# Kernel tuning notes

Hardware: AMD Instinct MI355X
Metric: run time of the kernel (lower is better)

The kernel has to match this reference:

```python
import jax, jax.numpy as jnp
import numpy as np

B, N, M, D = 8, 1024, 2048, 1024


def setup_inputs() -> dict:
    key = jax.random.key(0)
    k1, k2, k3 = jax.random.split(key, 3)
    text_features = jax.random.normal(k1, (B, N, D), dtype=jnp.float32)
    audio_features = jax.random.normal(k2, (B, M, D), dtype=jnp.float32)
    sigma = jnp.ones((1,), dtype=jnp.float32)  # learnable bandwidth, initial_sigma=1.0
    # audio lengths in [M//4, M) so no softmax row is fully masked
    audio_lengths = jnp.maximum(
        jax.random.randint(k3, (B,), 0, M), M // 4
    ).astype(jnp.int32)
    return {
        "text_features": text_features,
        "audio_features": audio_features,
        "sigma": sigma,
        "audio_lengths": audio_lengths,
    }


def reference(text_features, audio_features, sigma, audio_lengths):
    b, n, d = text_features.shape
    m = audio_features.shape[1]
    s = jnp.abs(sigma[0]) + 1e-8

    # QK^T / sqrt(d)  -> (B, N, M)
    scores = jnp.einsum("bnd,bmd->bnm", text_features, audio_features) / jnp.sqrt(
        jnp.float32(d)
    )

    # Gaussian relative positional bias: -|i/N - j/M|^2 / (2 sigma^2)
    text_pos = jnp.arange(n, dtype=jnp.float32) / n    # (N,)
    audio_pos = jnp.arange(m, dtype=jnp.float32) / m   # (M,)
    d_rel = jnp.abs(text_pos[:, None] - audio_pos[None, :])  # (N, M)
    scores = scores - d_rel**2 / (2.0 * s * s)

    # mask padded audio positions per batch element
    valid = jnp.arange(m)[None, :] < audio_lengths[:, None]  # (B, M) bool
    scores = jnp.where(valid[:, None, :], scores, -jnp.inf)

    attention_weights = jax.nn.softmax(scores, axis=-1)  # (B, N, M)
    enhanced = jnp.einsum("bnm,bmd->bnd", attention_weights, audio_features)
    return enhanced, attention_weights
```

## Files before the change

### kernel.cpp

```cpp
#include <hip/hip_runtime.h>
#include <hip/hip_bf16.h>

#define BB 8
#define NN 1024
#define MM 2048
#define DD 1024

typedef __attribute__((ext_vector_type(8))) __bf16 bfrag8;
typedef __attribute__((ext_vector_type(4))) float ffrag4;

__device__ __forceinline__ unsigned short f2bf(float f) {
  union { float f; unsigned u; } x; x.f = f;
  unsigned r = x.u + 0x7FFFu + ((x.u >> 16) & 1u);
  return (unsigned short)(r >> 16);
}

__device__ __forceinline__ void gload_lds16(const unsigned short* g, unsigned short* l) {
  __builtin_amdgcn_global_load_lds(
      (const __attribute__((address_space(1))) void*)g,
      (__attribute__((address_space(3))) void*)l, 16, 0, 0);
}


__global__ __launch_bounds__(256) void ta_cvtQ(const float* __restrict__ Q,
                                               unsigned short* __restrict__ Qbf) {
  int t = blockIdx.x * 256 + threadIdx.x;
  const float4* src = reinterpret_cast<const float4*>(Q) + t * 2;
  float4 a = src[0], b = src[1];
  ushort4 lo = { f2bf(a.x), f2bf(a.y), f2bf(a.z), f2bf(a.w) };
  ushort4 hi = { f2bf(b.x), f2bf(b.y), f2bf(b.z), f2bf(b.w) };
  ushort4* dst = reinterpret_cast<ushort4*>(Qbf) + t * 2;
  dst[0] = lo; dst[1] = hi;
}

#define TSTR 68
__global__ __launch_bounds__(256) void ta_trans(const float* __restrict__ V,
                                                unsigned short* __restrict__ Kbf,
                                                unsigned short* __restrict__ VT) {
  const int dt = blockIdx.x;
  const int mt = blockIdx.y;
  const int b  = blockIdx.z;
  const int t  = threadIdx.x;
  __shared__ unsigned short Tls[64 * TSTR];

  const float* Vb = V + (size_t)b * MM * DD + (size_t)(mt * 64) * DD + dt * 64;
#pragma unroll
  for (int it = 0; it < 4; ++it) {
    int slot = t + 256 * it;
    int row  = slot >> 4;
    int c4   = slot & 15;
    float4 a = *reinterpret_cast<const float4*>(Vb + (size_t)row * DD + c4 * 4);
    ushort4 h = { f2bf(a.x), f2bf(a.y), f2bf(a.z), f2bf(a.w) };
    *reinterpret_cast<ushort4*>(&Tls[row * TSTR + c4 * 4]) = h;
  }
  __syncthreads();

  unsigned short* Kb = Kbf + (size_t)b * MM * DD + (size_t)(mt * 64) * DD + dt * 64;
  unsigned short* Vt = VT  + (size_t)b * DD * MM + (size_t)(dt * 64) * MM + mt * 64;
#pragma unroll
  for (int it = 0; it < 4; ++it) {
    int slot = t + 256 * it;
    int row  = slot >> 4;
    int c4   = slot & 15;
    *reinterpret_cast<ushort4*>(Kb + (size_t)row * DD + c4 * 4) =
        *reinterpret_cast<const ushort4*>(&Tls[row * TSTR + c4 * 4]);
    ushort4 tv = { Tls[(c4 * 4 + 0) * TSTR + row],
                   Tls[(c4 * 4 + 1) * TSTR + row],
                   Tls[(c4 * 4 + 2) * TSTR + row],
                   Tls[(c4 * 4 + 3) * TSTR + row] };
    *reinterpret_cast<ushort4*>(Vt + (size_t)row * MM + c4 * 4) = tv;
  }
}

__global__ void ta_zero(float* __restrict__ sums) {
  int t = blockIdx.x * 256 + threadIdx.x;
  if (t < BB * NN) sums[t] = 0.0f;
}

__global__ __launch_bounds__(256) void ta_gemm1m(
    const unsigned short* __restrict__ Q,
    const unsigned short* __restrict__ K,
    const float* __restrict__ sigma,
    const int* __restrict__ lens,
    unsigned short* __restrict__ Ebf,
    float* __restrict__ rowsum)
{
  const int bj = blockIdx.x, bi = blockIdx.y, b = blockIdx.z;
  const int t = threadIdx.x;
  const int lane = t & 63;
  const int w  = t >> 6;
  const int wi = w >> 1, wj = w & 1;

  __shared__ unsigned short As[4096];
  __shared__ unsigned short Bs[4096];

  const unsigned short* Qb = Q + (size_t)b * NN * DD + (size_t)(bi * 128) * DD;
  const unsigned short* Kb = K + (size_t)b * MM * DD + (size_t)(bj * 128) * DD;

  ffrag4 acc[4][4] = {};

  const int r    = lane & 15;
  const int quad = lane >> 4;
  const int rc  = lane >> 2;
  const int sc8 = (((lane & 3) ^ ((rc ^ (rc >> 2)) & 3)) << 3);
  const int swz = (r ^ (r >> 2)) & 3;

  for (int k0 = 0; k0 < DD; k0 += 32) {
#pragma unroll
    for (int n = 0; n < 2; ++n) {
      int g = w * 2 + n;
      int row = g * 16 + rc;
      gload_lds16(Qb + (size_t)row * DD + k0 + sc8, &As[g * 512]);
      gload_lds16(Kb + (size_t)row * DD + k0 + sc8, &Bs[g * 512]);
    }
    __syncthreads();

    bfrag8 af[4], bf[4];
#pragma unroll
    for (int ti = 0; ti < 4; ++ti)
      af[ti] = *reinterpret_cast<const bfrag8*>(&As[(wi * 64 + ti * 16 + r) * 32 + ((quad ^ swz) << 3)]);
#pragma unroll
    for (int tj = 0; tj < 4; ++tj)
      bf[tj] = *reinterpret_cast<const bfrag8*>(&Bs[(wj * 64 + tj * 16 + r) * 32 + ((quad ^ swz) << 3)]);

#pragma unroll
    for (int ti = 0; ti < 4; ++ti)
#pragma unroll
      for (int tj = 0; tj < 4; ++tj)
        acc[ti][tj] = __builtin_amdgcn_mfma_f32_16x16x32_bf16(af[ti], bf[tj], acc[ti][tj], 0, 0, 0);
    __syncthreads();
  }

  const float s = fabsf(sigma[0]) + 1e-8f;
  const float inv2s2 = 1.0f / (2.0f * s * s);
  const int len = lens[b];
  unsigned short* Erow = Ebf + (size_t)b * NN * MM;
  float* sums = rowsum + (size_t)b * NN;
  const int ibase = bi * 128 + wi * 64;
  const int jbase = bj * 128 + wj * 64;

#pragma unroll
  for (int ti = 0; ti < 4; ++ti) {
#pragma unroll
    for (int v = 0; v < 4; ++v) {
      int i = ibase + ti * 16 + quad * 4 + v;
      float psum = 0.0f;
#pragma unroll
      for (int tj = 0; tj < 4; ++tj) {
        int j = jbase + tj * 16 + r;
        float e = 0.0f;
        if (j < len) {
          float dr = (float)i * (1.0f / (float)NN) - (float)j * (1.0f / (float)MM);
          float sc = acc[ti][tj][v] * 0.03125f - dr * dr * inv2s2;
          e = __expf(fminf(sc, 30.0f));
        }
        psum += e;
        Erow[(size_t)i * MM + j] = f2bf(e);
      }
      psum += __shfl_xor(psum, 1);
      psum += __shfl_xor(psum, 2);
      psum += __shfl_xor(psum, 4);
      psum += __shfl_xor(psum, 8);
      if (r == 0) atomicAdd(&sums[i], psum);
    }
  }
}

__global__ __launch_bounds__(256) void ta_normA(
    const unsigned short* __restrict__ Ebf,
    const float* __restrict__ sums,
    float* __restrict__ attn)
{
  int t = blockIdx.x * 256 + threadIdx.x;
  int row = t >> 8;
  const float inv = 1.0f / fmaxf(sums[row], 1e-30f);
  uint4 x = *(reinterpret_cast<const uint4*>(Ebf) + t);
  unsigned u[4] = { x.x, x.y, x.z, x.w };
  float o[8];
#pragma unroll
  for (int k = 0; k < 4; ++k) {
    union { unsigned u; float f; } lo, hi;
    lo.u = u[k] << 16; hi.u = u[k] & 0xFFFF0000u;
    o[2 * k]     = lo.f * inv;
    o[2 * k + 1] = hi.f * inv;
  }
  float4* dst = reinterpret_cast<float4*>(attn) + t * 2;
  float4 f0 = { o[0], o[1], o[2], o[3] };
  float4 f1 = { o[4], o[5], o[6], o[7] };
  dst[0] = f0; dst[1] = f1;
}

__global__ __launch_bounds__(256) void ta_gemm2m(
    const unsigned short* __restrict__ E,
    const unsigned short* __restrict__ VT,
    const float* __restrict__ rowsum,
    float* __restrict__ O)
{
  const int bd = blockIdx.x, bi = blockIdx.y, b = blockIdx.z;
  const int t = threadIdx.x;
  const int lane = t & 63;
  const int w  = t >> 6;
  const int wi = w >> 1, wj = w & 1;

  __shared__ unsigned short As[4096];
  __shared__ unsigned short Bs[4096];

  const unsigned short* Eb = E  + (size_t)b * NN * MM + (size_t)(bi * 128) * MM;
  const unsigned short* Vb = VT + (size_t)b * DD * MM + (size_t)(bd * 128) * MM;

  ffrag4 acc[4][4] = {};

  const int r    = lane & 15;
  const int quad = lane >> 4;
  const int rc  = lane >> 2;
  const int sc8 = (((lane & 3) ^ ((rc ^ (rc >> 2)) & 3)) << 3);
  const int swz = (r ^ (r >> 2)) & 3;

  for (int k0 = 0; k0 < MM; k0 += 32) {
#pragma unroll
    for (int n = 0; n < 2; ++n) {
      int g = w * 2 + n;
      int row = g * 16 + rc;
      gload_lds16(Eb + (size_t)row * MM + k0 + sc8, &As[g * 512]);
      gload_lds16(Vb + (size_t)row * MM + k0 + sc8, &Bs[g * 512]);
    }
    __syncthreads();

    bfrag8 af[4], bf[4];
#pragma unroll
    for (int ti = 0; ti < 4; ++ti)
      af[ti] = *reinterpret_cast<const bfrag8*>(&As[(wi * 64 + ti * 16 + r) * 32 + ((quad ^ swz) << 3)]);
#pragma unroll
    for (int tj = 0; tj < 4; ++tj)
      bf[tj] = *reinterpret_cast<const bfrag8*>(&Bs[(wj * 64 + tj * 16 + r) * 32 + ((quad ^ swz) << 3)]);

#pragma unroll
    for (int ti = 0; ti < 4; ++ti)
#pragma unroll
      for (int tj = 0; tj < 4; ++tj)
        acc[ti][tj] = __builtin_amdgcn_mfma_f32_16x16x32_bf16(af[ti], bf[tj], acc[ti][tj], 0, 0, 0);
    __syncthreads();
  }

  float* Ob = O + (size_t)b * NN * DD;
  const float* rs = rowsum + (size_t)b * NN;
  const int ibase = bi * 128 + wi * 64;
  const int dbase = bd * 128 + wj * 64;
#pragma unroll
  for (int ti = 0; ti < 4; ++ti) {
#pragma unroll
    for (int v = 0; v < 4; ++v) {
      int i = ibase + ti * 16 + quad * 4 + v;
      float inv = 1.0f / fmaxf(rs[i], 1e-30f);
#pragma unroll
      for (int tj = 0; tj < 4; ++tj) {
        int d = dbase + tj * 16 + r;
        Ob[(size_t)i * DD + d] = acc[ti][tj][v] * inv;
      }
    }
  }
}

#define LDA 40
__global__ __launch_bounds__(256) void tb_gemm1e(
    const float* __restrict__ Q, const float* __restrict__ K,
    const float* __restrict__ sigma, const int* __restrict__ lens,
    float* __restrict__ attn, float* __restrict__ rowsum)
{
  const int bj = blockIdx.x, bi = blockIdx.y, b = blockIdx.z;
  const int t = threadIdx.x;
  const int lane = t & 63;
  const int w = t >> 6;
  const int wi = w >> 1, wj = w & 1;
  __shared__ unsigned short Als[128 * LDA];
  __shared__ unsigned short Bls[128 * LDA];
  const float* Qb = Q + (size_t)b * NN * DD + (size_t)(bi * 128) * DD;
  const float* Kb = K + (size_t)b * MM * DD + (size_t)(bj * 128) * DD;
  ffrag4 acc[4][4] = {};
  const int r = lane & 15;
  const int koff = (lane >> 4) * 8;
  for (int k0 = 0; k0 < DD; k0 += 32) {
#pragma unroll
    for (int it = 0; it < 4; ++it) {
      int slot = t + 256 * it;
      int row = slot >> 3, c4 = slot & 7;
      float4 qa = *reinterpret_cast<const float4*>(Qb + (size_t)row * DD + k0 + c4 * 4);
      float4 ka = *reinterpret_cast<const float4*>(Kb + (size_t)row * DD + k0 + c4 * 4);
      ushort4 qh = { f2bf(qa.x), f2bf(qa.y), f2bf(qa.z), f2bf(qa.w) };
      ushort4 kh = { f2bf(ka.x), f2bf(ka.y), f2bf(ka.z), f2bf(ka.w) };
      *reinterpret_cast<ushort4*>(&Als[row * LDA + c4 * 4]) = qh;
      *reinterpret_cast<ushort4*>(&Bls[row * LDA + c4 * 4]) = kh;
    }
    __syncthreads();
    bfrag8 af[4], bf[4];
#pragma unroll
    for (int ti = 0; ti < 4; ++ti)
      af[ti] = *reinterpret_cast<const bfrag8*>(&Als[(wi * 64 + ti * 16 + r) * LDA + koff]);
#pragma unroll
    for (int tj = 0; tj < 4; ++tj)
      bf[tj] = *reinterpret_cast<const bfrag8*>(&Bls[(wj * 64 + tj * 16 + r) * LDA + koff]);
#pragma unroll
    for (int ti = 0; ti < 4; ++ti)
#pragma unroll
      for (int tj = 0; tj < 4; ++tj)
        acc[ti][tj] = __builtin_amdgcn_mfma_f32_16x16x32_bf16(af[ti], bf[tj], acc[ti][tj], 0, 0, 0);
    __syncthreads();
  }
  const float s = fabsf(sigma[0]) + 1e-8f;
  const float inv2s2 = 1.0f / (2.0f * s * s);
  const int len = lens[b];
  float* Prow = attn + (size_t)b * NN * MM;
  float* sums = rowsum + (size_t)b * NN;
  const int ibase = bi * 128 + wi * 64;
  const int jbase = bj * 128 + wj * 64;
  const int quad = lane >> 4;
#pragma unroll
  for (int ti = 0; ti < 4; ++ti) {
#pragma unroll
    for (int v = 0; v < 4; ++v) {
      int i = ibase + ti * 16 + quad * 4 + v;
      float psum = 0.0f;
#pragma unroll
      for (int tj = 0; tj < 4; ++tj) {
        int j = jbase + tj * 16 + r;
        float e = 0.0f;
        if (j < len) {
          float dr = (float)i * (1.0f / (float)NN) - (float)j * (1.0f / (float)MM);
          float sc = acc[ti][tj][v] * 0.03125f - dr * dr * inv2s2;
          e = __expf(fminf(sc, 30.0f));
        }
        psum += e;
        Prow[(size_t)i * MM + j] = e;
      }
      psum += __shfl_xor(psum, 1);
      psum += __shfl_xor(psum, 2);
      psum += __shfl_xor(psum, 4);
      psum += __shfl_xor(psum, 8);
      if (r == 0) atomicAdd(&sums[i], psum);
    }
  }
}

__global__ __launch_bounds__(256) void tb_norm(float* __restrict__ attn,
                                               const float* __restrict__ sums) {
  int t = blockIdx.x * 256 + threadIdx.x;
  int row = t >> 9;
  const float inv = 1.0f / fmaxf(sums[row], 1e-30f);
  float4* p = reinterpret_cast<float4*>(attn) + t;
  float4 x = *p;
  x.x *= inv; x.y *= inv; x.z *= inv; x.w *= inv;
  *p = x;
}

__global__ __launch_bounds__(256) void tb_gemm2(
    const float* __restrict__ P, const float* __restrict__ V, float* __restrict__ O)
{
  const int bd = blockIdx.x, bi = blockIdx.y, b = blockIdx.z;
  const int t = threadIdx.x;
  const int lane = t & 63;
  const int w = t >> 6;
  const int wi = w >> 1, wj = w & 1;
  __shared__ unsigned short Pls[128 * LDA];
  __shared__ unsigned short Vls[128 * LDA];
  const float* Pb = P + (size_t)b * NN * MM + (size_t)(bi * 128) * MM;
  const float* Vb = V + (size_t)b * MM * DD + bd * 128;
  ffrag4 acc[4][4] = {};
  const int r = lane & 15;
  const int koff = (lane >> 4) * 8;
  const int vd = t & 127;
  const int vmb = (t >> 7) * 16;
  for (int k0 = 0; k0 < MM; k0 += 32) {
#pragma unroll
    for (int it = 0; it < 4; ++it) {
      int slot = t + 256 * it;
      int row = slot >> 3, c4 = slot & 7;
      float4 pa = *reinterpret_cast<const float4*>(Pb + (size_t)row * MM + k0 + c4 * 4);
      ushort4 ph = { f2bf(pa.x), f2bf(pa.y), f2bf(pa.z), f2bf(pa.w) };
      *reinterpret_cast<ushort4*>(&Pls[row * LDA + c4 * 4]) = ph;
    }
    union { unsigned short h[16]; uint4 q[2]; } hv;
#pragma unroll
    for (int i = 0; i < 16; ++i)
      hv.h[i] = f2bf(Vb[(size_t)(k0 + vmb + i) * DD + vd]);
    *reinterpret_cast<uint4*>(&Vls[vd * LDA + vmb]) = hv.q[0];
    *reinterpret_cast<uint4*>(&Vls[vd * LDA + vmb + 8]) = hv.q[1];
    __syncthreads();
    bfrag8 af[4], bf[4];
#pragma unroll
    for (int ti = 0; ti < 4; ++ti)
      af[ti] = *reinterpret_cast<const bfrag8*>(&Pls[(wi * 64 + ti * 16 + r) * LDA + koff]);
#pragma unroll
    for (int tj = 0; tj < 4; ++tj)
      bf[tj] = *reinterpret_cast<const bfrag8*>(&Vls[(wj * 64 + tj * 16 + r) * LDA + koff]);
#pragma unroll
    for (int ti = 0; ti < 4; ++ti)
#pragma unroll
      for (int tj = 0; tj < 4; ++tj)
        acc[ti][tj] = __builtin_amdgcn_mfma_f32_16x16x32_bf16(af[ti], bf[tj], acc[ti][tj], 0, 0, 0);
    __syncthreads();
  }
  float* Ob = O + (size_t)b * NN * DD;
  const int ibase = bi * 128 + wi * 64;
  const int dbase = bd * 128 + wj * 64;
#pragma unroll
  for (int ti = 0; ti < 4; ++ti) {
#pragma unroll
    for (int tj = 0; tj < 4; ++tj) {
      int d = dbase + tj * 16 + r;
#pragma unroll
      for (int v = 0; v < 4; ++v) {
        int i = ibase + ti * 16 + (lane >> 4) * 4 + v;
        Ob[(size_t)i * DD + d] = acc[ti][tj][v];
      }
    }
  }
}

extern "C" void kernel_launch(void* const* d_in, const int* in_sizes, int n_in,
                              void* d_out, int out_size, void* d_ws, size_t ws_size,
                              hipStream_t stream) {
  const float* text  = (const float*)d_in[0];
  const float* audio = (const float*)d_in[1];
  const float* sigma = (const float*)d_in[2];
  const int*   lens  = (const int*)d_in[3];

  float* out = (float*)d_out;
  float* enhanced = out;
  float* attn = out + (size_t)BB * NN * DD;

  const size_t QBF  = (size_t)BB * NN * DD * 2;
  const size_t KBF  = (size_t)BB * MM * DD * 2;
  const size_t VTB  = (size_t)BB * DD * MM * 2;
  const size_t EBF  = (size_t)BB * NN * MM * 2;
  const size_t offQ = 65536;
  const size_t offK = offQ + QBF;
  const size_t offV = offK + KBF;
  const size_t offE = offV + VTB;
  const size_t need = offE + EBF;

  float* rowsum = (float*)d_ws;

  if (ws_size >= need) {
    unsigned short* Qbf = (unsigned short*)((char*)d_ws + offQ);
    unsigned short* Kbf = (unsigned short*)((char*)d_ws + offK);
    unsigned short* VT  = (unsigned short*)((char*)d_ws + offV);
    unsigned short* Ebf = (unsigned short*)((char*)d_ws + offE);

    ta_zero<<<dim3((BB * NN + 255) / 256), 256, 0, stream>>>(rowsum);
    ta_cvtQ<<<dim3(BB * NN * DD / 8 / 256), 256, 0, stream>>>(text, Qbf);
    ta_trans<<<dim3(DD / 64, MM / 64, BB), 256, 0, stream>>>(audio, Kbf, VT);
    ta_gemm1m<<<dim3(MM / 128, NN / 128, BB), 256, 0, stream>>>(Qbf, Kbf, sigma, lens, Ebf, rowsum);
    ta_normA<<<dim3(BB * NN * MM / 8 / 256), 256, 0, stream>>>(Ebf, rowsum, attn);
    ta_gemm2m<<<dim3(DD / 128, NN / 128, BB), 256, 0, stream>>>(Ebf, VT, rowsum, enhanced);
  } else {
    ta_zero<<<dim3((BB * NN + 255) / 256), 256, 0, stream>>>(rowsum);
    tb_gemm1e<<<dim3(MM / 128, NN / 128, BB), 256, 0, stream>>>(text, audio, sigma, lens, attn, rowsum);
    tb_norm<<<dim3(BB * NN * MM / 4 / 256), 256, 0, stream>>>(attn, rowsum);
    tb_gemm2<<<dim3(DD / 128, NN / 128, BB), 256, 0, stream>>>(attn, audio, enhanced);
  }
}
```

Before: 303.1 us.

## Rewrite both bf16 GEMMs with larger tiles, double-buffered async loads and ping-pong scheduling

New measurement: 280.4 us. -7.5%, faster.

```diff
diff --git a/kernel.cpp b/kernel.cpp
--- a/kernel.cpp
+++ b/kernel.cpp
@@ -19,6 +19,23 @@
   __builtin_amdgcn_global_load_lds(
       (const __attribute__((address_space(1))) void*)g,
       (__attribute__((address_space(3))) void*)l, 16, 0, 0);
+}
+
+#define SCHED0() __builtin_amdgcn_sched_barrier(0)
+#define P_PRE()  do { SCHED0(); __builtin_amdgcn_s_barrier();                 \
+                      asm volatile("s_waitcnt lgkmcnt(0)" ::: "memory");      \
+                      SCHED0(); __builtin_amdgcn_s_setprio(1); } while (0)
+#define P_POST() do { __builtin_amdgcn_s_setprio(0); SCHED0();                \
+                      __builtin_amdgcn_s_barrier(); } while (0)
+
+#define MFMA16x16x32 __builtin_amdgcn_mfma_f32_16x16x32_bf16
+
+__device__ __forceinline__ void stage_half(const unsigned short* gbase, int ldk,
+                                           unsigned short* ldst,
+                                           int w, int r0, int slog) {
+  const unsigned short* g = gbase + (size_t)(w * 8 + r0) * ldk + slog;
+  gload_lds16(g, ldst + w * 512);
+  gload_lds16(g + (size_t)64 * ldk, ldst + 4096 + w * 512);
 }
 
 
@@ -77,7 +94,7 @@
   if (t < BB * NN) sums[t] = 0.0f;
 }
 
-__global__ __launch_bounds__(256) void ta_gemm1m(
+__global__ __launch_bounds__(512, 2) void ta_gemm1x(
     const unsigned short* __restrict__ Q,
     const unsigned short* __restrict__ K,
     const float* __restrict__ sigma,
@@ -87,71 +104,142 @@
 {
   const int bj = blockIdx.x, bi = blockIdx.y, b = blockIdx.z;
   const int t = threadIdx.x;
-  const int lane = t & 63;
-  const int w  = t >> 6;
-  const int wi = w >> 1, wj = w & 1;
-
-  __shared__ unsigned short As[4096];
-  __shared__ unsigned short Bs[4096];
-
-  const unsigned short* Qb = Q + (size_t)b * NN * DD + (size_t)(bi * 128) * DD;
-  const unsigned short* Kb = K + (size_t)b * MM * DD + (size_t)(bj * 128) * DD;
-
-  ffrag4 acc[4][4] = {};
-
-  const int r    = lane & 15;
-  const int quad = lane >> 4;
-  const int rc  = lane >> 2;
-  const int sc8 = (((lane & 3) ^ ((rc ^ (rc >> 2)) & 3)) << 3);
-  const int swz = (r ^ (r >> 2)) & 3;
-
-  for (int k0 = 0; k0 < DD; k0 += 32) {
-#pragma unroll
-    for (int n = 0; n < 2; ++n) {
-      int g = w * 2 + n;
-      int row = g * 16 + rc;
-      gload_lds16(Qb + (size_t)row * DD + k0 + sc8, &As[g * 512]);
-      gload_lds16(Kb + (size_t)row * DD + k0 + sc8, &Bs[g * 512]);
-    }
-    __syncthreads();
-
-    bfrag8 af[4], bf[4];
-#pragma unroll
-    for (int ti = 0; ti < 4; ++ti)
-      af[ti] = *reinterpret_cast<const bfrag8*>(&As[(wi * 64 + ti * 16 + r) * 32 + ((quad ^ swz) << 3)]);
-#pragma unroll
-    for (int tj = 0; tj < 4; ++tj)
-      bf[tj] = *reinterpret_cast<const bfrag8*>(&Bs[(wj * 64 + tj * 16 + r) * 32 + ((quad ^ swz) << 3)]);
-
-#pragma unroll
-    for (int ti = 0; ti < 4; ++ti)
-#pragma unroll
-      for (int tj = 0; tj < 4; ++tj)
-        acc[ti][tj] = __builtin_amdgcn_mfma_f32_16x16x32_bf16(af[ti], bf[tj], acc[ti][tj], 0, 0, 0);
-    __syncthreads();
-  }
-
-  const float s = fabsf(sigma[0]) + 1e-8f;
-  const float inv2s2 = 1.0f / (2.0f * s * s);
+  const int lane = t & 63, w = t >> 6;
+  const int wr = w >> 2, wc = w & 3;
+  __shared__ unsigned short S[65536];
+
+  const unsigned short* Qb = Q + (size_t)b * NN * DD + (size_t)(bi * 256) * DD;
+  const unsigned short* Kb = K + (size_t)b * MM * DD + (size_t)(bj * 256) * DD;
+
+  const int r  = lane & 15, qd = lane >> 4;
+  const int r0 = (lane >> 3) & 7;
+  const int slog = ((lane & 7) ^ r0) << 3;
+  const int cs0 = ((qd)     ^ (r & 7)) << 3;
+  const int cs1 = ((4 + qd) ^ (r & 7)) << 3;
+
+  ffrag4 acc[8][4] = {};
+
+  {
+    unsigned short* T0 = &S[0];
+    stage_half(Qb,                        DD, T0,          w, r0, slog);
+    stage_half(Qb + (size_t)128 * DD,     DD, T0 + 8192,   w, r0, slog);
+    stage_half(Kb,                        DD, T0 + 16384,  w, r0, slog);
+    stage_half(Kb + (size_t)128 * DD,     DD, T0 + 24576,  w, r0, slog);
+    unsigned short* T1 = &S[32768];
+    stage_half(Qb + 64,                    DD, T1,          w, r0, slog);
+    stage_half(Qb + (size_t)128 * DD + 64, DD, T1 + 8192,   w, r0, slog);
+    stage_half(Kb + 64,                    DD, T1 + 16384,  w, r0, slog);
+    stage_half(Kb + (size_t)128 * DD + 64, DD, T1 + 24576,  w, r0, slog);
+    asm volatile("s_waitcnt vmcnt(8)" ::: "memory");
+    __builtin_amdgcn_s_barrier();
+  }
+
+  for (int kt = 0; kt < 16; ++kt) {
+    const int p = kt & 1;
+    unsigned short* Ab = &S[p * 32768 + wr * 8192];
+    unsigned short* Bb = &S[p * 32768 + 16384 + (wc >> 1) * 8192];
+    const int brb = (wc & 1) * 64;
+    bfrag8 af[4][2], bf0[2][2], bf1[2][2];
+
+#pragma unroll
+    for (int mi = 0; mi < 4; ++mi) {
+      const unsigned short* a = &Ab[(mi * 16 + r) * 64];
+      af[mi][0] = *reinterpret_cast<const bfrag8*>(a + cs0);
+      af[mi][1] = *reinterpret_cast<const bfrag8*>(a + cs1);
+    }
+#pragma unroll
+    for (int jj = 0; jj < 2; ++jj) {
+      const unsigned short* bp = &Bb[(brb + jj * 16 + r) * 64];
+      bf0[jj][0] = *reinterpret_cast<const bfrag8*>(bp + cs0);
+      bf0[jj][1] = *reinterpret_cast<const bfrag8*>(bp + cs1);
+    }
+    P_PRE();
+#pragma unroll
+    for (int mi = 0; mi < 4; ++mi)
+#pragma unroll
+      for (int jj = 0; jj < 2; ++jj) {
+        acc[mi][jj] = MFMA16x16x32(af[mi][0], bf0[jj][0], acc[mi][jj], 0, 0, 0);
+        acc[mi][jj] = MFMA16x16x32(af[mi][1], bf0[jj][1], acc[mi][jj], 0, 0, 0);
+      }
+    P_POST();
+
+#pragma unroll
+    for (int jj = 0; jj < 2; ++jj) {
+      const unsigned short* bp = &Bb[(brb + (2 + jj) * 16 + r) * 64];
+      bf1[jj][0] = *reinterpret_cast<const bfrag8*>(bp + cs0);
+      bf1[jj][1] = *reinterpret_cast<const bfrag8*>(bp + cs1);
+    }
+    P_PRE();
+#pragma unroll
+    for (int mi = 0; mi < 4; ++mi)
+#pragma unroll
+      for (int jj = 0; jj < 2; ++jj) {
+        acc[mi][2 + jj] = MFMA16x16x32(af[mi][0], bf1[jj][0], acc[mi][2 + jj], 0, 0, 0);
+        acc[mi][2 + jj] = MFMA16x16x32(af[mi][1], bf1[jj][1], acc[mi][2 + jj], 0, 0, 0);
+      }
+    P_POST();
+
+#pragma unroll
+    for (int mi = 0; mi < 4; ++mi) {
+      const unsigned short* a = &Ab[((mi + 4) * 16 + r) * 64];
+      af[mi][0] = *reinterpret_cast<const bfrag8*>(a + cs0);
+      af[mi][1] = *reinterpret_cast<const bfrag8*>(a + cs1);
+    }
+    if (kt + 2 < 16) {
+      unsigned short* Dst = &S[p * 32768 + 16384];
+      stage_half(Kb + (kt + 2) * 64,                    DD, Dst,        w, r0, slog);
+      stage_half(Kb + (size_t)128 * DD + (kt + 2) * 64, DD, Dst + 8192, w, r0, slog);
+    }
+    P_PRE();
+#pragma unroll
+    for (int mi = 0; mi < 4; ++mi)
+#pragma unroll
+      for (int jj = 0; jj < 2; ++jj) {
+        acc[4 + mi][2 + jj] = MFMA16x16x32(af[mi][0], bf1[jj][0], acc[4 + mi][2 + jj], 0, 0, 0);
+        acc[4 + mi][2 + jj] = MFMA16x16x32(af[mi][1], bf1[jj][1], acc[4 + mi][2 + jj], 0, 0, 0);
+      }
+    P_POST();
+
+    if (kt + 2 < 16) {
+      unsigned short* Dst = &S[p * 32768];
+      stage_half(Qb + (kt + 2) * 64,                    DD, Dst,        w, r0, slog);
+      stage_half(Qb + (size_t)128 * DD + (kt + 2) * 64, DD, Dst + 8192, w, r0, slog);
+    }
+    P_PRE();
+#pragma unroll
+    for (int mi = 0; mi < 4; ++mi)
+#pragma unroll
+      for (int jj = 0; jj < 2; ++jj) {
+        acc[4 + mi][jj] = MFMA16x16x32(af[mi][0], bf0[jj][0], acc[4 + mi][jj], 0, 0, 0);
+        acc[4 + mi][jj] = MFMA16x16x32(af[mi][1], bf0[jj][1], acc[4 + mi][jj], 0, 0, 0);
+      }
+    __builtin_amdgcn_s_setprio(0);
+    SCHED0();
+    if (kt + 2 < 16)      { asm volatile("s_waitcnt vmcnt(8)" ::: "memory"); }
+    else if (kt + 1 < 16) { asm volatile("s_waitcnt vmcnt(0)" ::: "memory"); }
+    __builtin_amdgcn_s_barrier();
+  }
+
+  const float sg = fabsf(sigma[0]) + 1e-8f;
+  const float inv2s2 = 1.0f / (2.0f * sg * sg);
   const int len = lens[b];
   unsigned short* Erow = Ebf + (size_t)b * NN * MM;
   float* sums = rowsum + (size_t)b * NN;
-  const int ibase = bi * 128 + wi * 64;
-  const int jbase = bj * 128 + wj * 64;
-
-#pragma unroll
-  for (int ti = 0; ti < 4; ++ti) {
+  const int ibase = bi * 256 + wr * 128;
+  const int jbase = bj * 256 + wc * 64;
+#pragma unroll
+  for (int mi = 0; mi < 8; ++mi) {
 #pragma unroll
     for (int v = 0; v < 4; ++v) {
-      int i = ibase + ti * 16 + quad * 4 + v;
+      int i = ibase + mi * 16 + qd * 4 + v;
       float psum = 0.0f;
 #pragma unroll
-      for (int tj = 0; tj < 4; ++tj) {
-        int j = jbase + tj * 16 + r;
+      for (int nj = 0; nj < 4; ++nj) {
+        int j = jbase + nj * 16 + r;
         float e = 0.0f;
         if (j < len) {
           float dr = (float)i * (1.0f / (float)NN) - (float)j * (1.0f / (float)MM);
-          float sc = acc[ti][tj][v] * 0.03125f - dr * dr * inv2s2;
+          float sc = acc[mi][nj][v] * 0.03125f - dr * dr * inv2s2;
           e = __expf(fminf(sc, 30.0f));
         }
         psum += e;
@@ -162,6 +250,144 @@
       psum += __shfl_xor(psum, 4);
       psum += __shfl_xor(psum, 8);
       if (r == 0) atomicAdd(&sums[i], psum);
+    }
+  }
+}
+
+__global__ __launch_bounds__(512, 2) void ta_gemm2x(
+    const unsigned short* __restrict__ E,
+    const unsigned short* __restrict__ VT,
+    const float* __restrict__ rowsum,
+    float* __restrict__ O)
+{
+  const int bd = blockIdx.x, bi = blockIdx.y, b = blockIdx.z;
+  const int t = threadIdx.x;
+  const int lane = t & 63, w = t >> 6;
+  const int wr = w >> 2, wc = w & 3;
+  __shared__ unsigned short S[49152];
+
+  const unsigned short* Eb = E  + (size_t)b * NN * MM + (size_t)(bi * 128) * MM;
+  const unsigned short* Vb = VT + (size_t)b * DD * MM + (size_t)(bd * 256) * MM;
+
+  const int r  = lane & 15, qd = lane >> 4;
+  const int r0 = (lane >> 3) & 7;
+  const int slog = ((lane & 7) ^ r0) << 3;
+  const int cs0 = ((qd)     ^ (r & 7)) << 3;
+  const int cs1 = ((4 + qd) ^ (r & 7)) << 3;
+
+  ffrag4 acc[4][4] = {};
+
+  {
+    stage_half(Eb,                        MM, &S[0],     w, r0, slog);
+    stage_half(Vb,                        MM, &S[8192],  w, r0, slog);
+    stage_half(Vb + (size_t)128 * MM,     MM, &S[16384], w, r0, slog);
+    stage_half(Eb + 64,                    MM, &S[24576],         w, r0, slog);
+    stage_half(Vb + 64,                    MM, &S[24576 + 8192],  w, r0, slog);
+    stage_half(Vb + (size_t)128 * MM + 64, MM, &S[24576 + 16384], w, r0, slog);
+    asm volatile("s_waitcnt vmcnt(6)" ::: "memory");
+    __builtin_amdgcn_s_barrier();
+  }
+
+  for (int kt = 0; kt < 32; ++kt) {
+    const int p = kt & 1;
+    unsigned short* Ab = &S[p * 24576];
+    unsigned short* Bb = &S[p * 24576 + 8192 + (wc >> 1) * 8192];
+    const int arb = wr * 64;
+    const int brb = (wc & 1) * 64;
+    bfrag8 af[2][2], bf0[2][2], bf1[2][2];
+
+#pragma unroll
+    for (int mi = 0; mi < 2; ++mi) {
+      const unsigned short* a = &Ab[(arb + mi * 16 + r) * 64];
+      af[mi][0] = *reinterpret_cast<const bfrag8*>(a + cs0);
+      af[mi][1] = *reinterpret_cast<const bfrag8*>(a + cs1);
+    }
+#pragma unroll
+    for (int jj = 0; jj < 2; ++jj) {
+      const unsigned short* bp = &Bb[(brb + jj * 16 + r) * 64];
+      bf0[jj][0] = *reinterpret_cast<const bfrag8*>(bp + cs0);
+      bf0[jj][1] = *reinterpret_cast<const bfrag8*>(bp + cs1);
+    }
+    P_PRE();
+#pragma unroll
+    for (int mi = 0; mi < 2; ++mi)
+#pragma unroll
+      for (int jj = 0; jj < 2; ++jj) {
+        acc[mi][jj] = MFMA16x16x32(af[mi][0], bf0[jj][0], acc[mi][jj], 0, 0, 0);
+        acc[mi][jj] = MFMA16x16x32(af[mi][1], bf0[jj][1], acc[mi][jj], 0, 0, 0);
+      }
+    P_POST();
+
+#pragma unroll
+    for (int jj = 0; jj < 2; ++jj) {
+      const unsigned short* bp = &Bb[(brb + (2 + jj) * 16 + r) * 64];
+      bf1[jj][0] = *reinterpret_cast<const bfrag8*>(bp + cs0);
+      bf1[jj][1] = *reinterpret_cast<const bfrag8*>(bp + cs1);
+    }
+    P_PRE();
+#pragma unroll
+    for (int mi = 0; mi < 2; ++mi)
+#pragma unroll
+      for (int jj = 0; jj < 2; ++jj) {
+        acc[mi][2 + jj] = MFMA16x16x32(af[mi][0], bf1[jj][0], acc[mi][2 + jj], 0, 0, 0);
+        acc[mi][2 + jj] = MFMA16x16x32(af[mi][1], bf1[jj][1], acc[mi][2 + jj], 0, 0, 0);
+      }
+    P_POST();
+
+#pragma unroll
+    for (int mi = 0; mi < 2; ++mi) {
+      const unsigned short* a = &Ab[(arb + (mi + 2) * 16 + r) * 64];
+      af[mi][0] = *reinterpret_cast<const bfrag8*>(a + cs0);
+      af[mi][1] = *reinterpret_cast<const bfrag8*>(a + cs1);
+    }
+    if (kt + 2 < 32) {
+      unsigned short* Dst = &S[p * 24576 + 8192];
+      stage_half(Vb + (kt + 2) * 64,                    MM, Dst,        w, r0, slog);
+      stage_half(Vb + (size_t)128 * MM + (kt + 2) * 64, MM, Dst + 8192, w, r0, slog);
+    }
+    P_PRE();
+#pragma unroll
+    for (int mi = 0; mi < 2; ++mi)
+#pragma unroll
+      for (int jj = 0; jj < 2; ++jj) {
+        acc[2 + mi][2 + jj] = MFMA16x16x32(af[mi][0], bf1[jj][0], acc[2 + mi][2 + jj], 0, 0, 0);
+        acc[2 + mi][2 + jj] = MFMA16x16x32(af[mi][1], bf1[jj][1], acc[2 + mi][2 + jj], 0, 0, 0);
+      }
+    P_POST();
+
+    if (kt + 2 < 32) {
+      stage_half(Eb + (kt + 2) * 64, MM, &S[p * 24576], w, r0, slog);
+    }
+    P_PRE();
+#pragma unroll
+    for (int mi = 0; mi < 2; ++mi)
+#pragma unroll
+      for (int jj = 0; jj < 2; ++jj) {
+        acc[2 + mi][jj] = MFMA16x16x32(af[mi][0], bf0[jj][0], acc[2 + mi][jj], 0, 0, 0);
+        acc[2 + mi][jj] = MFMA16x16x32(af[mi][1], bf0[jj][1], acc[2 + mi][jj], 0, 0, 0);
+      }
+    __builtin_amdgcn_s_setprio(0);
+    SCHED0();
+    if (kt + 2 < 32)      { asm volatile("s_waitcnt vmcnt(6)" ::: "memory"); }
+    else if (kt + 1 < 32) { asm volatile("s_waitcnt vmcnt(0)" ::: "memory"); }
+    __builtin_amdgcn_s_barrier();
+  }
+
+  float* Ob = O + (size_t)b * NN * DD;
+  const float* rs = rowsum + (size_t)b * NN;
+  const int ibase = bi * 128 + wr * 64;
+  const int dbase = bd * 256 + wc * 64;
+#pragma unroll
+  for (int mi = 0; mi < 4; ++mi) {
+#pragma unroll
+    for (int v = 0; v < 4; ++v) {
+      int i = ibase + mi * 16 + qd * 4 + v;
+      float inv = 1.0f / fmaxf(rs[i], 1e-30f);
+#pragma unroll
+      for (int nj = 0; nj < 4; ++nj) {
+        int d = dbase + nj * 16 + r;
+        Ob[(size_t)i * DD + d] = acc[mi][nj][v] * inv;
+      }
     }
   }
 }
@@ -188,77 +414,6 @@
   float4 f0 = { o[0], o[1], o[2], o[3] };
   float4 f1 = { o[4], o[5], o[6], o[7] };
   dst[0] = f0; dst[1] = f1;
-}
-
-__global__ __launch_bounds__(256) void ta_gemm2m(
-    const unsigned short* __restrict__ E,
-    const unsigned short* __restrict__ VT,
-    const float* __restrict__ rowsum,
-    float* __restrict__ O)
-{
-  const int bd = blockIdx.x, bi = blockIdx.y, b = blockIdx.z;
-  const int t = threadIdx.x;
-  const int lane = t & 63;
-  const int w  = t >> 6;
-  const int wi = w >> 1, wj = w & 1;
-
-  __shared__ unsigned short As[4096];
-  __shared__ unsigned short Bs[4096];
-
-  const unsigned short* Eb = E  + (size_t)b * NN * MM + (size_t)(bi * 128) * MM;
-  const unsigned short* Vb = VT + (size_t)b * DD * MM + (size_t)(bd * 128) * MM;
-
-  ffrag4 acc[4][4] = {};
-
-  const int r    = lane & 15;
-  const int quad = lane >> 4;
-  const int rc  = lane >> 2;
-  const int sc8 = (((lane & 3) ^ ((rc ^ (rc >> 2)) & 3)) << 3);
-  const int swz = (r ^ (r >> 2)) & 3;
-
-  for (int k0 = 0; k0 < MM; k0 += 32) {
-#pragma unroll
-    for (int n = 0; n < 2; ++n) {
-      int g = w * 2 + n;
-      int row = g * 16 + rc;
-      gload_lds16(Eb + (size_t)row * MM + k0 + sc8, &As[g * 512]);
-      gload_lds16(Vb + (size_t)row * MM + k0 + sc8, &Bs[g * 512]);
-    }
-    __syncthreads();
-
-    bfrag8 af[4], bf[4];
-#pragma unroll
-    for (int ti = 0; ti < 4; ++ti)
-      af[ti] = *reinterpret_cast<const bfrag8*>(&As[(wi * 64 + ti * 16 + r) * 32 + ((quad ^ swz) << 3)]);
-#pragma unroll
-    for (int tj = 0; tj < 4; ++tj)
-      bf[tj] = *reinterpret_cast<const bfrag8*>(&Bs[(wj * 64 + tj * 16 + r) * 32 + ((quad ^ swz) << 3)]);
-
-#pragma unroll
-    for (int ti = 0; ti < 4; ++ti)
-#pragma unroll
-      for (int tj = 0; tj < 4; ++tj)
-        acc[ti][tj] = __builtin_amdgcn_mfma_f32_16x16x32_bf16(af[ti], bf[tj], acc[ti][tj], 0, 0, 0);
-    __syncthreads();
-  }
-
-  float* Ob = O + (size_t)b * NN * DD;
-  const float* rs = rowsum + (size_t)b * NN;
-  const int ibase = bi * 128 + wi * 64;
-  const int dbase = bd * 128 + wj * 64;
-#pragma unroll
-  for (int ti = 0; ti < 4; ++ti) {
-#pragma unroll
-    for (int v = 0; v < 4; ++v) {
-      int i = ibase + ti * 16 + quad * 4 + v;
-      float inv = 1.0f / fmaxf(rs[i], 1e-30f);
-#pragma unroll
-      for (int tj = 0; tj < 4; ++tj) {
-        int d = dbase + tj * 16 + r;
-        Ob[(size_t)i * DD + d] = acc[ti][tj][v] * inv;
-      }
-    }
-  }
 }
 
 #define LDA 40
@@ -303,7 +458,7 @@
     for (int ti = 0; ti < 4; ++ti)
 #pragma unroll
       for (int tj = 0; tj < 4; ++tj)
-        acc[ti][tj] = __builtin_amdgcn_mfma_f32_16x16x32_bf16(af[ti], bf[tj], acc[ti][tj], 0, 0, 0);
+        acc[ti][tj] = MFMA16x16x32(af[ti], bf[tj], acc[ti][tj], 0, 0, 0);
     __syncthreads();
   }
   const float s = fabsf(sigma[0]) + 1e-8f;
@@ -396,7 +551,7 @@
     for (int ti = 0; ti < 4; ++ti)
 #pragma unroll
       for (int tj = 0; tj < 4; ++tj)
-        acc[ti][tj] = __builtin_amdgcn_mfma_f32_16x16x32_bf16(af[ti], bf[tj], acc[ti][tj], 0, 0, 0);
+        acc[ti][tj] = MFMA16x16x32(af[ti], bf[tj], acc[ti][tj], 0, 0, 0);
     __syncthreads();
   }
   float* Ob = O + (size_t)b * NN * DD;
@@ -449,9 +604,9 @@
     ta_zero<<<dim3((BB * NN + 255) / 256), 256, 0, stream>>>(rowsum);
     ta_cvtQ<<<dim3(BB * NN * DD / 8 / 256), 256, 0, stream>>>(text, Qbf);
     ta_trans<<<dim3(DD / 64, MM / 64, BB), 256, 0, stream>>>(audio, Kbf, VT);
-    ta_gemm1m<<<dim3(MM / 128, NN / 128, BB), 256, 0, stream>>>(Qbf, Kbf, sigma, lens, Ebf, rowsum);
+    ta_gemm1x<<<dim3(MM / 256, NN / 256, BB), 512, 0, stream>>>(Qbf, Kbf, sigma, lens, Ebf, rowsum);
     ta_normA<<<dim3(BB * NN * MM / 8 / 256), 256, 0, stream>>>(Ebf, rowsum, attn);
-    ta_gemm2m<<<dim3(DD / 128, NN / 128, BB), 256, 0, stream>>>(Ebf, VT, rowsum, enhanced);
+    ta_gemm2x<<<dim3(DD / 256, NN / 128, BB), 512, 0, stream>>>(Ebf, VT, rowsum, enhanced);
   } else {
     ta_zero<<<dim3((BB * NN + 255) / 256), 256, 0, stream>>>(rowsum);
     tb_gemm1e<<<dim3(MM / 128, NN / 128, BB), 256, 0, stream>>>(text, audio, sigma, lens, attn, rowsum);
```
